# Optimization experiments

Measured on AMD Instinct MI355X. Metric: run time of the kernel, lower is better.

Reference implementation:

```python
import jax, jax.numpy as jnp
import numpy as np

N_HEADS = 16


def _apply_rope(x, cos, sin):
    # x: [B, H, S, hd]; cos/sin: [>=S, hd/2]
    S = x.shape[2]
    cos = cos[None, None, :S]
    sin = sin[None, None, :S]
    x1, x2 = x[..., ::2], x[..., 1::2]
    # interleaved rotate, matching torch stack(...).flatten(-2)
    return jnp.stack([x1 * cos - x2 * sin, x1 * sin + x2 * cos], axis=-1).reshape(x.shape)


def setup_inputs() -> dict:
    key = jax.random.key(0)
    B, S, D = 2, 2048, 1024
    hd = D // N_HEADS
    k1, k2, k3 = jax.random.split(key, 3)
    x = jax.random.normal(k1, (B, S, D), dtype=jnp.float32)
    # standard RoPE tables (theta=10000)
    inv_freq = 1.0 / (10000.0 ** (np.arange(0, hd, 2, dtype=np.float32) / hd))  # [hd/2]
    freqs = np.outer(np.arange(S, dtype=np.float32), inv_freq)  # [S, hd/2]
    rope_cos = jnp.asarray(np.cos(freqs), dtype=jnp.float32)
    rope_sin = jnp.asarray(np.sin(freqs), dtype=jnp.float32)
    W_qkv = jax.random.normal(k2, (D, 3 * D), dtype=jnp.float32) * (D ** -0.5)
    W_out = jax.random.normal(k3, (D, D), dtype=jnp.float32) * (D ** -0.5)
    return {"x": x, "rope_cos": rope_cos, "rope_sin": rope_sin, "W_qkv": W_qkv, "W_out": W_out}


def reference(x, rope_cos, rope_sin, W_qkv, W_out):
    B, S, D = x.shape
    H = N_HEADS
    hd = D // H
    qkv = (x @ W_qkv).reshape(B, S, 3, H, hd)  # fused QKV projection
    q = qkv[:, :, 0].transpose(0, 2, 1, 3)  # [B,H,S,hd]
    k = qkv[:, :, 1].transpose(0, 2, 1, 3)
    v = qkv[:, :, 2].transpose(0, 2, 1, 3)
    q = _apply_rope(q, rope_cos, rope_sin)
    k = _apply_rope(k, rope_cos, rope_sin)
    scale = hd ** -0.5
    scores = jnp.einsum('bhqd,bhkd->bhqk', q, k) * scale  # [B,H,S,S]
    causal = jnp.tril(jnp.ones((S, S), dtype=bool))
    scores = jnp.where(causal, scores, jnp.finfo(scores.dtype).min)
    attn = jax.nn.softmax(scores, axis=-1)
    out = jnp.einsum('bhqk,bhkd->bhqd', attn, v)  # [B,H,S,hd]
    out = out.transpose(0, 2, 1, 3).reshape(B, S, D)
    return out @ W_out  # dropout is identity in eval mode
```

## Files before the change

### kernel.cpp

```cpp
#include <hip/hip_runtime.h>
#include <hip/hip_bf16.h>
#include <stdint.h>

typedef short bf16x8 __attribute__((ext_vector_type(8)));
typedef short bf16x4 __attribute__((ext_vector_type(4)));
typedef float f32x4 __attribute__((ext_vector_type(4)));

#define HD 64
#define NH 16
#define SEQ 2048
#define BATCH 2
#define DM 1024
#define TOK (BATCH * SEQ)

__device__ __forceinline__ unsigned short f2bf(float f) {
    union { float f; unsigned u; } a; a.f = f;
    unsigned r = a.u + 0x7fffu + ((a.u >> 16) & 1u);
    return (unsigned short)(r >> 16);
}
__device__ __forceinline__ float bf2f(unsigned short u) {
    union { unsigned u; float f; } a; a.u = ((unsigned)u) << 16;
    return a.f;
}

__device__ __forceinline__ unsigned pkbf16(float a, float b) {
    union { __hip_bfloat162 h; unsigned u; } cv;
    cv.h = __float22bfloat162_rn(make_float2(a, b));
    return cv.u;
}

__device__ __forceinline__ float fexp2(float x) {
#if __has_builtin(__builtin_amdgcn_exp2f)
    return __builtin_amdgcn_exp2f(x);
#else
    return exp2f(x);
#endif
}
__device__ __forceinline__ float frcp(float x) {
#if __has_builtin(__builtin_amdgcn_rcpf)
    return __builtin_amdgcn_rcpf(x);
#else
    return 1.0f / x;
#endif
}

__device__ __forceinline__ f32x4 mfma16(bf16x4 a, bf16x4 b, f32x4 c) {
#if defined(__HIP_DEVICE_COMPILE__)
    return __builtin_amdgcn_mfma_f32_16x16x16bf16_1k(a, b, c, 0, 0, 0);
#else
    (void)a; (void)b;
    return c;
#endif
}

__device__ __forceinline__ void gld_lds16(const unsigned short* g, unsigned short* l) {
#if __has_builtin(__builtin_amdgcn_global_load_lds)
    __builtin_amdgcn_global_load_lds(
        (const __attribute__((address_space(1))) unsigned int*)g,
        (__attribute__((address_space(3))) unsigned int*)l, 16, 0, 0);
#else
    *(bf16x8*)l = *(const bf16x8*)g;
#endif
}

__global__ void __launch_bounds__(256) k_prep(const float* __restrict__ x,
                                              unsigned short* __restrict__ xb,
                                              const float* __restrict__ wqkv,
                                              unsigned short* __restrict__ wqkvt,
                                              const float* __restrict__ wout,
                                              unsigned short* __restrict__ woutt) {
    int bid = blockIdx.x;
    int tid = threadIdx.x;
    if (bid < 4096) {
        int i = (bid * 256 + tid) * 4;
        float4 v = *(const float4*)(x + i);
        union { ushort4 v; unsigned short s[4]; } o;
        o.s[0] = f2bf(v.x); o.s[1] = f2bf(v.y); o.s[2] = f2bf(v.z); o.s[3] = f2bf(v.w);
        *(ushort4*)(xb + i) = o.v;
        return;
    }
    const float* W; unsigned short* Wt; int N, t;
    if (bid < 7168) { W = wqkv; Wt = wqkvt; N = 3 * DM; t = bid - 4096; }
    else            { W = wout; Wt = woutt; N = DM;     t = bid - 7168; }
    int ntx = N >> 5;
    int bx = t % ntx, by = t / ntx;
    int tx = tid & 31, ty = tid >> 5;
    __shared__ float tile[32][33];
    for (int r = 0; r < 4; ++r) {
        int k = by * 32 + ty + r * 8;
        int n = bx * 32 + tx;
        tile[ty + r * 8][tx] = W[(size_t)k * N + n];
    }
    __syncthreads();
    for (int r = 0; r < 4; ++r) {
        int n = bx * 32 + ty + r * 8;
        int k = by * 32 + tx;
        Wt[(size_t)n * DM + k] = f2bf(tile[tx][ty + r * 8]);
    }
}

#define BKK 32

template <int MODE>
__device__ __forceinline__ void gemm_core(const unsigned short* __restrict__ A,
                                          const unsigned short* __restrict__ Bt,
                                          int K, int N,
                                          float* __restrict__ C,
                                          unsigned short* __restrict__ qbuf,
                                          unsigned short* __restrict__ kbuf,
                                          unsigned short* __restrict__ vt) {
    __shared__ unsigned short As0[128 * BKK];
    __shared__ unsigned short As1[128 * BKK];
    __shared__ unsigned short Bs0[128 * BKK];
    __shared__ unsigned short Bs1[128 * BKK];
    int tid = threadIdx.x;
    int lane = tid & 63, wave = tid >> 6;
    int row0 = blockIdx.y * 128;
    int col0 = blockIdx.x * 128;
    int wm = (wave >> 1) * 64, wn = (wave & 1) * 64;
    int fr = lane & 15;
    int quad = lane >> 4;

    f32x4 zero4 = {0.f, 0.f, 0.f, 0.f};
    f32x4 acc[4][4];
    for (int i = 0; i < 4; ++i)
        for (int j = 0; j < 4; ++j) acc[i][j] = zero4;

    auto stage = [&](unsigned short* Ad, unsigned short* Bd, int k0) {
        for (int i = 0; i < 2; ++i) {
            int s2 = i * 256 + tid;
            int r = s2 >> 2, kc = s2 & 3;
            int kk = (kc ^ (r & 3)) * 8;
            gld_lds16(A + (size_t)(row0 + r) * K + k0 + kk, Ad + (i * 256 + wave * 64) * 8);
            gld_lds16(Bt + (size_t)(col0 + r) * K + k0 + kk, Bd + (i * 256 + wave * 64) * 8);
        }
    };
    auto compute = [&](const unsigned short* Al, const unsigned short* Bl) {
        bf16x8 af[4], bf[4];
        for (int i = 0; i < 4; ++i) {
            int rr = wm + i * 16 + fr;
            af[i] = *(const bf16x8*)&Al[rr * BKK + ((quad ^ (rr & 3)) * 8)];
        }
        for (int j = 0; j < 4; ++j) {
            int rr = wn + j * 16 + fr;
            bf[j] = *(const bf16x8*)&Bl[rr * BKK + ((quad ^ (rr & 3)) * 8)];
        }
        for (int i = 0; i < 4; ++i)
            for (int j = 0; j < 4; ++j)
                acc[i][j] = __builtin_amdgcn_mfma_f32_16x16x32_bf16(af[i], bf[j], acc[i][j], 0, 0, 0);
    };

    stage(As0, Bs0, 0);
    __syncthreads();
    for (int k0 = 0; k0 < K; k0 += 2 * BKK) {
        if (k0 + BKK < K) stage(As1, Bs1, k0 + BKK);
        compute(As0, Bs0);
        __syncthreads();
        if (k0 + 2 * BKK < K) stage(As0, Bs0, k0 + 2 * BKK);
        compute(As1, Bs1);
        __syncthreads();
    }

    int rq = (lane >> 4) * 4;
    int cq = lane & 15;
    for (int i = 0; i < 4; ++i)
        for (int j = 0; j < 4; ++j)
            for (int reg = 0; reg < 4; ++reg) {
                int row = row0 + wm + i * 16 + rq + reg;
                int col = col0 + wn + j * 16 + cq;
                float v = acc[i][j][reg];
                if (MODE == 0) {
                    C[(size_t)row * N + col] = v;
                } else {
                    int which = col >> 10;
                    int hc = col & 1023;
                    int h = hc >> 6, d = hc & 63;
                    int b = row >> 11, s = row & (SEQ - 1);
                    int bh = b * NH + h;
                    unsigned short bv = f2bf(v);
                    if (which == 0)      qbuf[((size_t)bh * SEQ + s) * HD + d] = bv;
                    else if (which == 1) kbuf[((size_t)bh * SEQ + s) * HD + d] = bv;
                    else                 vt[((size_t)bh * HD + d) * SEQ + s] = bv;
                }
            }
}

__global__ void __launch_bounds__(256) k_gemm_qkv(const unsigned short* __restrict__ A,
                                                  const unsigned short* __restrict__ Bt,
                                                  unsigned short* __restrict__ qbuf,
                                                  unsigned short* __restrict__ kbuf,
                                                  unsigned short* __restrict__ vt) {
    gemm_core<1>(A, Bt, DM, 3 * DM, nullptr, qbuf, kbuf, vt);
}

__global__ void __launch_bounds__(256) k_gemm_out(const unsigned short* __restrict__ A,
                                                  const unsigned short* __restrict__ Bt,
                                                  float* __restrict__ C) {
    gemm_core<0>(A, Bt, DM, DM, C, nullptr, nullptr, nullptr);
}

__global__ void k_rope(unsigned short* __restrict__ qbuf, unsigned short* __restrict__ kbuf,
                       const float* __restrict__ cosb, const float* __restrict__ sinb) {
    int t = blockIdx.x * 256 + threadIdx.x;
    int c = t & 7;
    int row = (t >> 3) & 65535;
    int which = t >> 19;
    unsigned short* p = (which ? kbuf : qbuf) + (size_t)row * HD + c * 8;
    float sc = which ? 1.0f : (0.125f * 1.44269504f);
    int s = row & (SEQ - 1);
    const float* cs = cosb + s * 32 + c * 4;
    const float* sn = sinb + s * 32 + c * 4;
    bf16x8 v = *(const bf16x8*)p;
    bf16x8 o;
    for (int i = 0; i < 4; ++i) {
        float x1 = bf2f((unsigned short)v[2 * i]);
        float x2 = bf2f((unsigned short)v[2 * i + 1]);
        float cc = cs[i], ss = sn[i];
        o[2 * i]     = (short)f2bf((x1 * cc - x2 * ss) * sc);
        o[2 * i + 1] = (short)f2bf((x1 * ss + x2 * cc) * sc);
    }
    *(bf16x8*)p = o;
}

__global__ void __launch_bounds__(256, 4) k_attn(const unsigned short* __restrict__ qbuf,
                                                 const unsigned short* __restrict__ kbuf,
                                                 const unsigned short* __restrict__ vt,
                                                 unsigned short* __restrict__ obuf) {
    __shared__ unsigned short Ks0[64 * 64];
    __shared__ unsigned short Ks1[64 * 64];
    __shared__ unsigned short Vs0[64 * 64];
    __shared__ unsigned short Vs1[64 * 64];

    int tid = threadIdx.x;
    int lane = tid & 63, wave = tid >> 6;
    int bh = blockIdx.y;
    int b = bh >> 4, h = bh & 15;
    int qt = (int)gridDim.x - 1 - (int)blockIdx.x;
    int qb = qt * 64;
    int fr = lane & 15, quad = lane >> 4;
    int Qmin = qb + wave * 16;

    const unsigned short* Qb = qbuf + (size_t)bh * SEQ * HD;
    const unsigned short* Kb = kbuf + (size_t)bh * SEQ * HD;
    const unsigned short* Vb = vt + (size_t)bh * HD * SEQ;

    int qrow = Qmin + fr;
    bf16x8 qf0 = *(const bf16x8*)(Qb + (size_t)qrow * HD + quad * 8);
    bf16x8 qf1 = *(const bf16x8*)(Qb + (size_t)qrow * HD + 32 + quad * 8);

    f32x4 zero4 = {0.f, 0.f, 0.f, 0.f};
    f32x4 o[4];
    for (int j = 0; j < 4; ++j) o[j] = zero4;
    float l = 0.f;

    auto stage = [&](int kb, unsigned short* Kd, unsigned short* Vd) {
        for (int a = 0; a < 2; ++a) {
            int idx = a * 256 + tid;
            int r = idx >> 3;
            int lg = (idx & 7) ^ (r & 7);
            gld_lds16(Kb + (size_t)(kb + r) * HD + lg * 8, Kd + (a * 256 + wave * 64) * 8);
            gld_lds16(Vb + (size_t)r * SEQ + kb + lg * 8, Vd + (a * 256 + wave * 64) * 8);
        }
    };

    auto compute = [&](int kt, const unsigned short* Kd, const unsigned short* Vd) {
        int kb = kt * 64;
        int sw = fr & 7;
        f32x4 sg[4];
        for (int g = 0; g < 4; ++g) {
            int r = g * 16 + fr;
            bf16x8 ka = *(const bf16x8*)&Kd[r * 64 + ((quad ^ sw) * 8)];
            bf16x8 kc = *(const bf16x8*)&Kd[r * 64 + (((quad + 4) ^ sw) * 8)];
            f32x4 z = zero4;
            z = __builtin_amdgcn_mfma_f32_16x16x32_bf16(ka, qf0, z, 0, 0, 0);
            z = __builtin_amdgcn_mfma_f32_16x16x32_bf16(kc, qf1, z, 0, 0, 0);
            sg[g] = z;
        }
        if (kt == qt) {
            int q = Qmin + fr;
            for (int g = 0; g < 4; ++g)
                for (int reg = 0; reg < 4; ++reg)
                    if (kb + g * 16 + quad * 4 + reg > q) sg[g][reg] = -1e30f;
        }
        bf16x4 pf[4];
        for (int g = 0; g < 4; ++g) {
            float p0 = fexp2(sg[g][0]);
            float p1 = fexp2(sg[g][1]);
            float p2 = fexp2(sg[g][2]);
            float p3 = fexp2(sg[g][3]);
            l += (p0 + p1) + (p2 + p3);
            union { bf16x4 v; unsigned u[2]; } pc;
            pc.u[0] = pkbf16(p0, p1);
            pc.u[1] = pkbf16(p2, p3);
            pf[g] = pc.v;
        }
        for (int g = 0; g < 4; ++g)
            for (int db = 0; db < 4; ++db) {
                int d = db * 16 + fr;
                int pg = ((2 * g + (quad >> 1)) ^ sw) * 8 + (quad & 1) * 4;
                bf16x4 vf = *(const bf16x4*)&Vd[d * 64 + pg];
                o[db] = mfma16(pf[g], vf, o[db]);
            }
    };

    stage(0, Ks0, Vs0);
    __syncthreads();
    for (int kt = 0; kt <= qt; kt += 2) {
        if (kt + 1 <= qt) stage((kt + 1) * 64, Ks1, Vs1);
        compute(kt, Ks0, Vs0);
        __syncthreads();
        if (kt + 1 <= qt) {
            if (kt + 2 <= qt) stage((kt + 2) * 64, Ks0, Vs0);
            compute(kt + 1, Ks1, Vs1);
            __syncthreads();
        }
    }

    l += __shfl_xor(l, 16);
    l += __shfl_xor(l, 32);
    float linv[4];
    for (int reg = 0; reg < 4; ++reg)
        linv[reg] = frcp(__shfl(l, quad * 4 + reg));

    for (int db = 0; db < 4; ++db)
        for (int reg = 0; reg < 4; ++reg) {
            int s = Qmin + quad * 4 + reg;
            int d = db * 16 + fr;
            obuf[((size_t)(b * SEQ + s)) * DM + h * HD + d] = f2bf(o[db][reg] * linv[reg]);
        }
}

extern "C" void kernel_launch(void* const* d_in, const int* in_sizes, int n_in,
                              void* d_out, int out_size, void* d_ws, size_t ws_size,
                              hipStream_t stream) {
    const float* x    = (const float*)d_in[0];
    const float* rc   = (const float*)d_in[1];
    const float* rs   = (const float*)d_in[2];
    const float* wqkv = (const float*)d_in[3];
    const float* wout = (const float*)d_in[4];
    float* out = (float*)d_out;

    char* ws = (char*)d_ws;
    size_t off = 0;
    auto alloc = [&](size_t bytes) {
        char* p = ws + off;
        off += (bytes + 255) & ~(size_t)255;
        return p;
    };
    unsigned short* xb    = (unsigned short*)alloc((size_t)TOK * DM * 2);
    unsigned short* wqkvt = (unsigned short*)alloc((size_t)3 * DM * DM * 2);
    unsigned short* woutt = (unsigned short*)alloc((size_t)DM * DM * 2);
    unsigned short* qbuf  = (unsigned short*)alloc((size_t)BATCH * NH * SEQ * HD * 2);
    unsigned short* kbuf  = (unsigned short*)alloc((size_t)BATCH * NH * SEQ * HD * 2);
    unsigned short* vtb   = (unsigned short*)alloc((size_t)BATCH * NH * SEQ * HD * 2);
    unsigned short* obuf  = (unsigned short*)alloc((size_t)TOK * DM * 2);

    k_prep<<<8192, 256, 0, stream>>>(x, xb, wqkv, wqkvt, wout, woutt);
    k_gemm_qkv<<<dim3(3 * DM / 128, TOK / 128), 256, 0, stream>>>(xb, wqkvt, qbuf, kbuf, vtb);
    k_rope<<<4096, 256, 0, stream>>>(qbuf, kbuf, rc, rs);
    k_attn<<<dim3(SEQ / 64, BATCH * NH), 256, 0, stream>>>(qbuf, kbuf, vtb, obuf);
    k_gemm_out<<<dim3(DM / 128, TOK / 128), 256, 0, stream>>>(obuf, woutt, out);
}
```

Before: 197.1 us.

## Process two query sub-tiles per wave in attention to reuse K/V fragments

The attention kernel now runs 2 waves per block instead of 4, and each wave handles 32 query rows as two 16-row sub-tiles. K and V fragments are read from LDS once per key tile and reused for both sub-tiles, which halves LDS read traffic per query row. Staging loops are widened so the smaller block still fills the same K/V tiles. The cost is higher register pressure (doubled accumulators plus cached K/V fragments) and fewer waves per block, which may lower occupancy and latency hiding.

```diff
diff --git a/kernel.cpp b/kernel.cpp
--- a/kernel.cpp
+++ b/kernel.cpp
@@ -222,7 +222,7 @@
     *(bf16x8*)p = o;
 }
 
-__global__ void __launch_bounds__(256, 4) k_attn(const unsigned short* __restrict__ qbuf,
+__global__ void __launch_bounds__(128, 2) k_attn(const unsigned short* __restrict__ qbuf,
                                                  const unsigned short* __restrict__ kbuf,
                                                  const unsigned short* __restrict__ vt,
                                                  unsigned short* __restrict__ obuf) {
@@ -237,70 +237,82 @@
     int b = bh >> 4, h = bh & 15;
     int qt = (int)gridDim.x - 1 - (int)blockIdx.x;
     int qb = qt * 64;
-    int fr = lane & 15, quad = lane >> 4;
-    int Qmin = qb + wave * 16;
+    int fr = lane & 15, quad = lane >> 4, sw = fr & 7;
+    int Qmin = qb + wave * 32;
 
     const unsigned short* Qb = qbuf + (size_t)bh * SEQ * HD;
     const unsigned short* Kb = kbuf + (size_t)bh * SEQ * HD;
     const unsigned short* Vb = vt + (size_t)bh * HD * SEQ;
 
-    int qrow = Qmin + fr;
-    bf16x8 qf0 = *(const bf16x8*)(Qb + (size_t)qrow * HD + quad * 8);
-    bf16x8 qf1 = *(const bf16x8*)(Qb + (size_t)qrow * HD + 32 + quad * 8);
+    bf16x8 qf[2][2];
+    for (int s = 0; s < 2; ++s) {
+        int qrow = Qmin + s * 16 + fr;
+        qf[s][0] = *(const bf16x8*)(Qb + (size_t)qrow * HD + quad * 8);
+        qf[s][1] = *(const bf16x8*)(Qb + (size_t)qrow * HD + 32 + quad * 8);
+    }
 
     f32x4 zero4 = {0.f, 0.f, 0.f, 0.f};
-    f32x4 o[4];
-    for (int j = 0; j < 4; ++j) o[j] = zero4;
-    float l = 0.f;
+    f32x4 o[2][4];
+    for (int s = 0; s < 2; ++s)
+        for (int j = 0; j < 4; ++j) o[s][j] = zero4;
+    float l[2] = {0.f, 0.f};
 
     auto stage = [&](int kb, unsigned short* Kd, unsigned short* Vd) {
-        for (int a = 0; a < 2; ++a) {
-            int idx = a * 256 + tid;
+        for (int a = 0; a < 4; ++a) {
+            int idx = a * 128 + tid;
             int r = idx >> 3;
             int lg = (idx & 7) ^ (r & 7);
-            gld_lds16(Kb + (size_t)(kb + r) * HD + lg * 8, Kd + (a * 256 + wave * 64) * 8);
-            gld_lds16(Vb + (size_t)r * SEQ + kb + lg * 8, Vd + (a * 256 + wave * 64) * 8);
+            gld_lds16(Kb + (size_t)(kb + r) * HD + lg * 8, Kd + (a * 128 + wave * 64) * 8);
+            gld_lds16(Vb + (size_t)r * SEQ + kb + lg * 8, Vd + (a * 128 + wave * 64) * 8);
         }
     };
 
     auto compute = [&](int kt, const unsigned short* Kd, const unsigned short* Vd) {
         int kb = kt * 64;
-        int sw = fr & 7;
-        f32x4 sg[4];
+        bf16x8 ka[4], kc[4];
         for (int g = 0; g < 4; ++g) {
             int r = g * 16 + fr;
-            bf16x8 ka = *(const bf16x8*)&Kd[r * 64 + ((quad ^ sw) * 8)];
-            bf16x8 kc = *(const bf16x8*)&Kd[r * 64 + (((quad + 4) ^ sw) * 8)];
-            f32x4 z = zero4;
-            z = __builtin_amdgcn_mfma_f32_16x16x32_bf16(ka, qf0, z, 0, 0, 0);
-            z = __builtin_amdgcn_mfma_f32_16x16x32_bf16(kc, qf1, z, 0, 0, 0);
-            sg[g] = z;
-        }
-        if (kt == qt) {
-            int q = Qmin + fr;
-            for (int g = 0; g < 4; ++g)
-                for (int reg = 0; reg < 4; ++reg)
-                    if (kb + g * 16 + quad * 4 + reg > q) sg[g][reg] = -1e30f;
-        }
-        bf16x4 pf[4];
-        for (int g = 0; g < 4; ++g) {
-            float p0 = fexp2(sg[g][0]);
-            float p1 = fexp2(sg[g][1]);
-            float p2 = fexp2(sg[g][2]);
-            float p3 = fexp2(sg[g][3]);
-            l += (p0 + p1) + (p2 + p3);
-            union { bf16x4 v; unsigned u[2]; } pc;
-            pc.u[0] = pkbf16(p0, p1);
-            pc.u[1] = pkbf16(p2, p3);
-            pf[g] = pc.v;
-        }
+            ka[g] = *(const bf16x8*)&Kd[r * 64 + ((quad ^ sw) * 8)];
+            kc[g] = *(const bf16x8*)&Kd[r * 64 + (((quad + 4) ^ sw) * 8)];
+        }
+        bf16x4 vf[4][4];
         for (int g = 0; g < 4; ++g)
             for (int db = 0; db < 4; ++db) {
                 int d = db * 16 + fr;
                 int pg = ((2 * g + (quad >> 1)) ^ sw) * 8 + (quad & 1) * 4;
-                bf16x4 vf = *(const bf16x4*)&Vd[d * 64 + pg];
-                o[db] = mfma16(pf[g], vf, o[db]);
-            }
+                vf[g][db] = *(const bf16x4*)&Vd[d * 64 + pg];
+            }
+        for (int s = 0; s < 2; ++s) {
+            f32x4 sg[4];
+            for (int g = 0; g < 4; ++g) {
+                f32x4 z = zero4;
+                z = __builtin_amdgcn_mfma_f32_16x16x32_bf16(ka[g], qf[s][0], z, 0, 0, 0);
+                z = __builtin_amdgcn_mfma_f32_16x16x32_bf16(kc[g], qf[s][1], z, 0, 0, 0);
+                sg[g] = z;
+            }
+            int Qs = Qmin + s * 16;
+            if (kb + 63 > Qs) {
+                int q = Qs + fr;
+                for (int g = 0; g < 4; ++g)
+                    for (int reg = 0; reg < 4; ++reg)
+                        if (kb + g * 16 + quad * 4 + reg > q) sg[g][reg] = -1e30f;
+            }
+            bf16x4 pf[4];
+            for (int g = 0; g < 4; ++g) {
+                float p0 = fexp2(sg[g][0]);
+                float p1 = fexp2(sg[g][1]);
+                float p2 = fexp2(sg[g][2]);
+                float p3 = fexp2(sg[g][3]);
+                l[s] += (p0 + p1) + (p2 + p3);
+                union { bf16x4 v; unsigned u[2]; } pc;
+                pc.u[0] = pkbf16(p0, p1);
+                pc.u[1] = pkbf16(p2, p3);
+                pf[g] = pc.v;
+            }
+            for (int g = 0; g < 4; ++g)
+                for (int db = 0; db < 4; ++db)
+                    o[s][db] = mfma16(pf[g], vf[g][db], o[s][db]);
+        }
     };
 
     stage(0, Ks0, Vs0);
@@ -316,18 +328,21 @@
         }
     }
 
-    l += __shfl_xor(l, 16);
-    l += __shfl_xor(l, 32);
-    float linv[4];
-    for (int reg = 0; reg < 4; ++reg)
-        linv[reg] = frcp(__shfl(l, quad * 4 + reg));
-
-    for (int db = 0; db < 4; ++db)
-        for (int reg = 0; reg < 4; ++reg) {
-            int s = Qmin + quad * 4 + reg;
-            int d = db * 16 + fr;
-            obuf[((size_t)(b * SEQ + s)) * DM + h * HD + d] = f2bf(o[db][reg] * linv[reg]);
-        }
+    for (int s = 0; s < 2; ++s) {
+        float ll = l[s];
+        ll += __shfl_xor(ll, 16);
+        ll += __shfl_xor(ll, 32);
+        float linv[4];
+        for (int reg = 0; reg < 4; ++reg)
+            linv[reg] = frcp(__shfl(ll, quad * 4 + reg));
+        int Qs = Qmin + s * 16;
+        for (int db = 0; db < 4; ++db)
+            for (int reg = 0; reg < 4; ++reg) {
+                int row = Qs + quad * 4 + reg;
+                int d = db * 16 + fr;
+                obuf[((size_t)(b * SEQ + row)) * DM + h * HD + d] = f2bf(o[s][db][reg] * linv[reg]);
+            }
+    }
 }
 
 extern "C" void kernel_launch(void* const* d_in, const int* in_sizes, int n_in,
@@ -358,6 +373,6 @@
     k_prep<<<8192, 256, 0, stream>>>(x, xb, wqkv, wqkvt, wout, woutt);
     k_gemm_qkv<<<dim3(3 * DM / 128, TOK / 128), 256, 0, stream>>>(xb, wqkvt, qbuf, kbuf, vtb);
     k_rope<<<4096, 256, 0, stream>>>(qbuf, kbuf, rc, rs);
-    k_attn<<<dim3(SEQ / 64, BATCH * NH), 256, 0, stream>>>(qbuf, kbuf, vtb, obuf);
+    k_attn<<<dim3(SEQ / 64, BATCH * NH), 128, 0, stream>>>(qbuf, kbuf, vtb, obuf);
     k_gemm_out<<<dim3(DM / 128, TOK / 128), 256, 0, stream>>>(obuf, woutt, out);
 }
```

Measured after the change: 196.5 us. About the same (-0.3%).
